# Kernel optimization log

Hardware: AMD Instinct MI355X
Metric: run time of the kernel (lower is better)

## Reference

```python
import jax, jax.numpy as jnp
import numpy as np

N_NODES = 50000
N_EDGES = 800000
IN_CH, OUT_CH, HEADS = 64, 32, 4
NEG_SLOPE = 0.2
BN_EPS = 1e-5


def setup_inputs() -> dict:
    key = jax.random.key(0)
    ks = jax.random.split(key, 9)
    x = jax.random.normal(ks[0], (N_NODES, IN_CH), dtype=jnp.float32)
    pos = jax.random.uniform(ks[1], (N_NODES, 3), dtype=jnp.float32)
    edge_index = jax.random.randint(ks[2], (2, N_EDGES), 0, N_NODES, dtype=jnp.int64)
    s = 1.0 / np.sqrt(IN_CH)
    W_l = jax.random.normal(ks[3], (IN_CH, HEADS * OUT_CH), dtype=jnp.float32) * s
    W_r = jax.random.normal(ks[4], (IN_CH, HEADS * OUT_CH), dtype=jnp.float32) * s
    W_edge = jax.random.normal(ks[5], (3, HEADS * OUT_CH), dtype=jnp.float32) * 0.5
    att = jax.random.normal(ks[6], (HEADS, OUT_CH), dtype=jnp.float32) * (1.0 / np.sqrt(OUT_CH))
    bn_gamma = jax.random.uniform(ks[7], (HEADS * OUT_CH,), dtype=jnp.float32, minval=0.5, maxval=1.5)
    bn_beta = jax.random.normal(ks[8], (HEADS * OUT_CH,), dtype=jnp.float32) * 0.1
    return {"x": x, "pos": pos, "edge_index": edge_index, "W_l": W_l, "W_r": W_r,
            "W_edge": W_edge, "att": att, "bn_gamma": bn_gamma, "bn_beta": bn_beta}


def reference(x, pos, edge_index, W_l, W_r, W_edge, att, bn_gamma, bn_beta):
    N = x.shape[0]
    H, C = att.shape
    # source->target projections (GATv2: lin_l for source/messages, lin_r for target)
    xl = (x @ W_l).reshape(N, H, C)
    xr = (x @ W_r).reshape(N, H, C)
    src, dst = edge_index[0], edge_index[1]
    edge_attr = pos[src] - pos[dst]  # [E,3] relative position as edge feature
    # add self-loops with fill_value='mean' (PyG default)
    loop = jnp.arange(N)
    src = jnp.concatenate([src, loop])
    dst = jnp.concatenate([dst, loop])
    mean_attr = edge_attr.mean(axis=0, keepdims=True)  # [1,3]
    edge_attr = jnp.concatenate([edge_attr, jnp.broadcast_to(mean_attr, (N, 3))], axis=0)
    # per-edge GATv2 score: att . LeakyReLU(x_l[j] + x_r[i] + W_e e_ij)
    e_feat = (edge_attr @ W_edge).reshape(-1, H, C)
    msg = xl[src]                              # [Et,H,C] (reused for aggregation)
    e = msg + xr[dst] + e_feat
    e = jax.nn.leaky_relu(e, NEG_SLOPE)
    score = jnp.einsum('ehc,hc->eh', e, att)   # [Et,H]
    # segment softmax over destination node
    m = jax.ops.segment_max(score, dst, num_segments=N)
    score = jnp.exp(score - m[dst])
    denom = jax.ops.segment_sum(score, dst, num_segments=N)
    alpha = score / (denom[dst] + 1e-16)       # [Et,H]
    out = jax.ops.segment_sum(alpha[:, :, None] * msg, dst, num_segments=N)
    out = out.reshape(N, H * C)
    # BatchNorm over node dimension (training-mode batch statistics, PyG BatchNorm)
    mu = out.mean(axis=0)
    var = out.var(axis=0)
    return (out - mu) / jnp.sqrt(var + BN_EPS) * bn_gamma + bn_beta
```

## Files before the change

kernel.cpp:

```cpp
#include <hip/hip_runtime.h>
#include <hip/hip_bf16.h>

#define N_NODES 50000
#define IN_CH 64
#define HC 128
#define CAP 64
#define NEG_SLOPE 0.2f
#define BN_EPS 1e-5f


__global__ __launch_bounds__(256) void k_gemm(const float* __restrict__ x,
                                              const float* __restrict__ Wl,
                                              const float* __restrict__ Wr,
                                              unsigned int* __restrict__ xl_bf,
                                              float* __restrict__ xr_out,
                                              int* __restrict__ deg,
                                              int* __restrict__ ocnt,
                                              float* __restrict__ mean_sums,
                                              float* __restrict__ bn_sums,
                                              int* __restrict__ flag,
                                              const int* __restrict__ eidx) {
  {
    int gtid = blockIdx.x * 256 + threadIdx.x;
    if (gtid < N_NODES) { deg[gtid] = 1; ocnt[gtid] = 0; }
    if (gtid < 256) bn_sums[gtid] = 0.f;
    if (gtid < 3) mean_sums[gtid] = 0.f;
    if (blockIdx.x == 0 && threadIdx.x < 64) {
      int w = eidx[2 * threadIdx.x + 1];
      unsigned long long nz = __ballot(w != 0);
      if (threadIdx.x == 0) flag[0] = (nz == 0ULL) ? 1 : 0;
    }
  }

  __shared__ float xs[16][IN_CH];
  __shared__ __hip_bfloat162 wsm[IN_CH][128];
  const int t = threadIdx.x;
  const int row0 = blockIdx.x * 16;

  for (int i = 0; i < 32; ++i) {
    int k = i * 2 + (t >> 7);
    int p = t & 127;
    int cc = p * 2;
    float2 wv;
    if (cc < 128) wv = *(const float2*)(Wl + k * 128 + cc);
    else          wv = *(const float2*)(Wr + k * 128 + (cc - 128));
    wsm[k][p] = __float22bfloat162_rn(wv);
  }
  {
    int r = t >> 4, c4 = (t & 15) * 4;
    *(float4*)&xs[r][c4] = *(const float4*)(x + (row0 + r) * IN_CH + c4);
  }
  __syncthreads();

  const int ct = t & 63;
  const int rt = t >> 6;
  const int c4 = ct * 4;
  const int r4 = rt * 4;

  float acc[4][4];
  #pragma unroll
  for (int a = 0; a < 4; ++a)
    #pragma unroll
    for (int b = 0; b < 4; ++b) acc[a][b] = 0.f;

  #pragma unroll 8
  for (int k = 0; k < IN_CH; ++k) {
    uint2 wraw = *(const uint2*)&wsm[k][ct * 2];
    float2 f01 = __bfloat1622float2(*(__hip_bfloat162*)&wraw.x);
    float2 f23 = __bfloat1622float2(*(__hip_bfloat162*)&wraw.y);
    float wv[4] = {f01.x, f01.y, f23.x, f23.y};
    float xv[4] = {xs[r4][k], xs[r4 + 1][k], xs[r4 + 2][k], xs[r4 + 3][k]};
    #pragma unroll
    for (int a = 0; a < 4; ++a)
      #pragma unroll
      for (int b = 0; b < 4; ++b) acc[a][b] = fmaf(xv[a], wv[b], acc[a][b]);
  }

  #pragma unroll
  for (int a = 0; a < 4; ++a) {
    int row = row0 + r4 + a;
    if (c4 < 128) {
      __hip_bfloat162 b01 = __float22bfloat162_rn(make_float2(acc[a][0], acc[a][1]));
      __hip_bfloat162 b23 = __float22bfloat162_rn(make_float2(acc[a][2], acc[a][3]));
      uint2 u;
      u.x = *(unsigned int*)&b01;
      u.y = *(unsigned int*)&b23;
      *(uint2*)(xl_bf + row * 64 + (c4 >> 1)) = u;
    } else {
      float4 v = make_float4(acc[a][0], acc[a][1], acc[a][2], acc[a][3]);
      *(float4*)(xr_out + row * HC + (c4 - 128)) = v;
    }
  }
}

__global__ __launch_bounds__(256) void k_edges(const int* __restrict__ eidx,
                                               int* __restrict__ deg,
                                               int* __restrict__ ocnt,
                                               int* __restrict__ srcs,
                                               const int* __restrict__ flag,
                                               int E) {
  const bool w64 = flag[0] != 0;
  const int stride = gridDim.x * blockDim.x;
  const int npair = (E + 1) >> 1;
  for (int e2 = blockIdx.x * blockDim.x + threadIdx.x; e2 < npair; e2 += stride) {
    int e0 = e2 * 2;
    bool has1 = (e0 + 1) < E;
    int s0, s1, d0, d1;
    if (w64) {
      int4 sv = *(const int4*)(eidx + 2 * e0);
      int4 dv = *(const int4*)(eidx + 2 * E + 2 * e0);
      s0 = sv.x; s1 = sv.z; d0 = dv.x; d1 = dv.z;
    } else {
      int2 sv = *(const int2*)(eidx + e0);
      int2 dv = *(const int2*)(eidx + E + e0);
      s0 = sv.x; s1 = sv.y; d0 = dv.x; d1 = dv.y;
    }
    int o0 = atomicAdd(&deg[d0], 1);
    if (o0 < CAP) srcs[d0 * CAP + o0] = s0;
    atomicAdd(&ocnt[s0], 1);
    if (has1) {
      int o1 = atomicAdd(&deg[d1], 1);
      if (o1 < CAP) srcs[d1 * CAP + o1] = s1;
      atomicAdd(&ocnt[s1], 1);
    }
  }
}

__global__ __launch_bounds__(256) void k_nodemean(const float* __restrict__ pos,
                                                  const int* __restrict__ deg,
                                                  const int* __restrict__ ocnt,
                                                  float* __restrict__ mean_sums) {
  float sx = 0.f, sy = 0.f, sz = 0.f;
  const int stride = gridDim.x * blockDim.x;
  for (int n = blockIdx.x * blockDim.x + threadIdx.x; n < N_NODES; n += stride) {
    float net = (float)(ocnt[n] - (deg[n] - 1));
    sx = fmaf(pos[3 * n],     net, sx);
    sy = fmaf(pos[3 * n + 1], net, sy);
    sz = fmaf(pos[3 * n + 2], net, sz);
  }
  #pragma unroll
  for (int m = 1; m < 64; m <<= 1) {
    sx += __shfl_xor(sx, m); sy += __shfl_xor(sy, m); sz += __shfl_xor(sz, m);
  }
  __shared__ float red[4][3];
  int wave = threadIdx.x >> 6, lane = threadIdx.x & 63;
  if (lane == 0) { red[wave][0] = sx; red[wave][1] = sy; red[wave][2] = sz; }
  __syncthreads();
  if (threadIdx.x == 0) {
    float a = 0.f, b = 0.f, c = 0.f;
    for (int w = 0; w < 4; ++w) { a += red[w][0]; b += red[w][1]; c += red[w][2]; }
    unsafeAtomicAdd(&mean_sums[0], a);
    unsafeAtomicAdd(&mean_sums[1], b);
    unsafeAtomicAdd(&mean_sums[2], c);
  }
}

__device__ __forceinline__ void edge4(int s, float dx, float dy, float dz, bool valid,
                                      const unsigned int* __restrict__ xl_bf, int l5,
                                      float4 xr4, float4 at4, float4 w0, float4 w1, float4 w2,
                                      float& a0, float& a1, float& a2, float& a3, float& den) {
  uint2 raw = *(const uint2*)(xl_bf + (s << 6) + (l5 << 1));
  float2 x01 = __bfloat1622float2(*(__hip_bfloat162*)&raw.x);
  float2 x23 = __bfloat1622float2(*(__hip_bfloat162*)&raw.y);
  float t0 = x01.x + xr4.x; t0 = fmaf(dx, w0.x, t0); t0 = fmaf(dy, w1.x, t0); t0 = fmaf(dz, w2.x, t0);
  float t1 = x01.y + xr4.y; t1 = fmaf(dx, w0.y, t1); t1 = fmaf(dy, w1.y, t1); t1 = fmaf(dz, w2.y, t1);
  float t2 = x23.x + xr4.z; t2 = fmaf(dx, w0.z, t2); t2 = fmaf(dy, w1.z, t2); t2 = fmaf(dz, w2.z, t2);
  float t3 = x23.y + xr4.w; t3 = fmaf(dx, w0.w, t3); t3 = fmaf(dy, w1.w, t3); t3 = fmaf(dz, w2.w, t3);
  float l0 = fmaf(NEG_SLOPE, fminf(t0, 0.f), fmaxf(t0, 0.f));
  float l1 = fmaf(NEG_SLOPE, fminf(t1, 0.f), fmaxf(t1, 0.f));
  float l2 = fmaf(NEG_SLOPE, fminf(t2, 0.f), fmaxf(t2, 0.f));
  float l3 = fmaf(NEG_SLOPE, fminf(t3, 0.f), fmaxf(t3, 0.f));
  float sc = l0 * at4.x;
  sc = fmaf(l1, at4.y, sc); sc = fmaf(l2, at4.z, sc); sc = fmaf(l3, at4.w, sc);
  sc += __shfl_xor(sc, 1); sc += __shfl_xor(sc, 2); sc += __shfl_xor(sc, 4);
  float e = __expf(sc);
  float p = valid ? e : 0.f;
  den += p;
  a0 = fmaf(p, x01.x, a0); a1 = fmaf(p, x01.y, a1);
  a2 = fmaf(p, x23.x, a2); a3 = fmaf(p, x23.y, a3);
}

__global__ __launch_bounds__(256) void k_agg(const unsigned int* __restrict__ xl_bf,
                                             float* __restrict__ xr_out,
                                             const float* __restrict__ pos,
                                             const float* __restrict__ att,
                                             const float* __restrict__ We,
                                             const float* __restrict__ mean_sums,
                                             const int* __restrict__ srcs,
                                             const int* __restrict__ deg,
                                             float invE) {
  const int lane = threadIdx.x & 63;
  const int half = lane >> 5;
  const int l5 = lane & 31;
  const int c = l5 << 2;

  const float4 at4 = *(const float4*)(att + c);
  const float4 w0 = *(const float4*)(We + c);
  const float4 w1 = *(const float4*)(We + 128 + c);
  const float4 w2 = *(const float4*)(We + 256 + c);
  const float m0 = mean_sums[0] * invE;
  const float m1 = mean_sums[1] * invE;
  const float m2 = mean_sums[2] * invE;

  const int gw = blockIdx.x * 4 + (threadIdx.x >> 6);
  const int W = gridDim.x * 4;

  for (int i = gw; i < N_NODES; i += W) {
    const float4 xr4 = *(const float4*)(xr_out + i * HC + c);
    const float px = pos[3 * i], py = pos[3 * i + 1], pz = pos[3 * i + 2];
    const int di = min(deg[i], CAP);
    const int sreg = srcs[i * CAP + lane];
    float a0 = 0.f, a1 = 0.f, a2 = 0.f, a3 = 0.f, den = 0.f;

    {
      int sA = __shfl(sreg, 1);
      if (half == 0) sA = i;
      bool vA = half < di;
      if (!vA) sA = i;
      int jB = 2 + half;
      int sB = __shfl(sreg, jB);
      bool vB = jB < di;
      if (!vB) sB = i;
      float pax = pos[3 * sA], pay = pos[3 * sA + 1], paz = pos[3 * sA + 2];
      float pbx = pos[3 * sB], pby = pos[3 * sB + 1], pbz = pos[3 * sB + 2];
      float dxA = (half == 0) ? m0 : pax - px;
      float dyA = (half == 0) ? m1 : pay - py;
      float dzA = (half == 0) ? m2 : paz - pz;
      edge4(sA, dxA, dyA, dzA, vA, xl_bf, l5, xr4, at4, w0, w1, w2, a0, a1, a2, a3, den);
      edge4(sB, pbx - px, pby - py, pbz - pz, vB, xl_bf, l5, xr4, at4, w0, w1, w2, a0, a1, a2, a3, den);
    }

    for (int j = 4; j < di; j += 4) {
      int jA = j + half;
      int jB = j + 2 + half;
      int sA = __shfl(sreg, jA);
      int sB = __shfl(sreg, jB);
      bool vA = jA < di;
      bool vB = jB < di;
      if (!vA) sA = i;
      if (!vB) sB = i;
      float pax = pos[3 * sA], pay = pos[3 * sA + 1], paz = pos[3 * sA + 2];
      float pbx = pos[3 * sB], pby = pos[3 * sB + 1], pbz = pos[3 * sB + 2];
      edge4(sA, pax - px, pay - py, paz - pz, vA, xl_bf, l5, xr4, at4, w0, w1, w2, a0, a1, a2, a3, den);
      edge4(sB, pbx - px, pby - py, pbz - pz, vB, xl_bf, l5, xr4, at4, w0, w1, w2, a0, a1, a2, a3, den);
    }

    den += __shfl_xor(den, 32);
    a0 += __shfl_xor(a0, 32);
    a1 += __shfl_xor(a1, 32);
    a2 += __shfl_xor(a2, 32);
    a3 += __shfl_xor(a3, 32);

    float inv = 1.f / (den + 1e-16f);
    if (half == 0) {
      float4 o = make_float4(a0 * inv, a1 * inv, a2 * inv, a3 * inv);
      *(float4*)(xr_out + i * HC + c) = o;
    }
  }
}

__global__ __launch_bounds__(128) void k_bnstats(const float* __restrict__ out,
                                                 float* __restrict__ bn_sums) {
  int c = threadIdx.x;
  float s = 0.f, ss = 0.f;
  int r = blockIdx.x;
  const int g = gridDim.x;
  for (; r + g < N_NODES; r += 2 * g) {
    float v0 = out[r * HC + c];
    float v1 = out[(r + g) * HC + c];
    s += v0; ss = fmaf(v0, v0, ss);
    s += v1; ss = fmaf(v1, v1, ss);
  }
  if (r < N_NODES) {
    float v = out[r * HC + c];
    s += v; ss = fmaf(v, v, ss);
  }
  unsafeAtomicAdd(&bn_sums[c], s);
  unsafeAtomicAdd(&bn_sums[128 + c], ss);
}

__global__ __launch_bounds__(256) void k_bnapply(float* __restrict__ out,
                                                 const float* __restrict__ bn_sums,
                                                 const float* __restrict__ gamma,
                                                 const float* __restrict__ beta,
                                                 int n4) {
  const int stride = gridDim.x * blockDim.x;
  const float invN = 1.f / (float)N_NODES;
  for (int i = blockIdx.x * blockDim.x + threadIdx.x; i < n4; i += stride) {
    int c = (i & 31) * 4;
    float4 v = ((float4*)out)[i];
    float4 s = *(const float4*)(bn_sums + c);
    float4 q = *(const float4*)(bn_sums + 128 + c);
    float4 g = *(const float4*)(gamma + c);
    float4 b = *(const float4*)(beta + c);
    float mu, var, rstd;
    mu = s.x * invN; var = q.x * invN - mu * mu; rstd = rsqrtf(var + BN_EPS);
    v.x = (v.x - mu) * rstd * g.x + b.x;
    mu = s.y * invN; var = q.y * invN - mu * mu; rstd = rsqrtf(var + BN_EPS);
    v.y = (v.y - mu) * rstd * g.y + b.y;
    mu = s.z * invN; var = q.z * invN - mu * mu; rstd = rsqrtf(var + BN_EPS);
    v.z = (v.z - mu) * rstd * g.z + b.z;
    mu = s.w * invN; var = q.w * invN - mu * mu; rstd = rsqrtf(var + BN_EPS);
    v.w = (v.w - mu) * rstd * g.w + b.w;
    ((float4*)out)[i] = v;
  }
}

extern "C" void kernel_launch(void* const* d_in, const int* in_sizes, int n_in,
                              void* d_out, int out_size, void* d_ws, size_t ws_size,
                              hipStream_t stream) {
  const float* x     = (const float*)d_in[0];
  const float* pos   = (const float*)d_in[1];
  const int*   eidx  = (const int*)d_in[2];
  const float* Wl    = (const float*)d_in[3];
  const float* Wr    = (const float*)d_in[4];
  const float* We    = (const float*)d_in[5];
  const float* att   = (const float*)d_in[6];
  const float* gamma = (const float*)d_in[7];
  const float* beta  = (const float*)d_in[8];
  float* out = (float*)d_out;
  const int E = in_sizes[2] / 2;

  char* ws = (char*)d_ws;
  int*   flag      = (int*)(ws + 0);
  float* mean_sums = (float*)(ws + 64);
  float* bn_sums   = (float*)(ws + 1024);
  int*   deg       = (int*)(ws + 4096);
  int*   ocnt      = (int*)(ws + (1 << 18));
  int*   srcs      = (int*)(ws + (1 << 19));
  unsigned int* xl_bf = (unsigned int*)(ws + (1 << 24));

  k_gemm<<<N_NODES / 16, 256, 0, stream>>>(x, Wl, Wr, xl_bf, out,
                                           deg, ocnt, mean_sums, bn_sums, flag, eidx);
  k_edges<<<1024, 256, 0, stream>>>(eidx, deg, ocnt, srcs, flag, E);
  k_nodemean<<<128, 256, 0, stream>>>(pos, deg, ocnt, mean_sums);
  k_agg<<<2048, 256, 0, stream>>>(xl_bf, out, pos, att, We, mean_sums, srcs, deg,
                                  1.f / (float)E);
  k_bnstats<<<512, 128, 0, stream>>>(out, bn_sums);
  k_bnapply<<<512, 256, 0, stream>>>(out, bn_sums, gamma, beta, out_size / 4);
}
```

Measured before the change: 288.9 us.

## Fuse edge-attr mean into edge scatter kernel, drop out-degree counting

The per-source out-count atomics and the separate node-mean kernel are removed. The edge kernel now accumulates pos[src]-pos[dst] directly and reduces it into mean_sums, with each thread handling 8 edges using vectorized index loads and batched atomics. This removes one atomic per edge and one kernel launch, at the cost of 6 random pos gathers per edge, and it changes the float summation order of the mean.

```diff
diff --git a/kernel.cpp b/kernel.cpp
--- a/kernel.cpp
+++ b/kernel.cpp
@@ -15,14 +15,13 @@
                                               unsigned int* __restrict__ xl_bf,
                                               float* __restrict__ xr_out,
                                               int* __restrict__ deg,
-                                              int* __restrict__ ocnt,
                                               float* __restrict__ mean_sums,
                                               float* __restrict__ bn_sums,
                                               int* __restrict__ flag,
                                               const int* __restrict__ eidx) {
   {
     int gtid = blockIdx.x * 256 + threadIdx.x;
-    if (gtid < N_NODES) { deg[gtid] = 1; ocnt[gtid] = 0; }
+    if (gtid < N_NODES) deg[gtid] = 1;
     if (gtid < 256) bn_sums[gtid] = 0.f;
     if (gtid < 3) mean_sums[gtid] = 0.f;
     if (blockIdx.x == 0 && threadIdx.x < 64) {
@@ -94,50 +93,62 @@
 }
 
 __global__ __launch_bounds__(256) void k_edges(const int* __restrict__ eidx,
+                                               const float* __restrict__ pos,
                                                int* __restrict__ deg,
-                                               int* __restrict__ ocnt,
                                                int* __restrict__ srcs,
+                                               float* __restrict__ mean_sums,
                                                const int* __restrict__ flag,
                                                int E) {
   const bool w64 = flag[0] != 0;
-  const int stride = gridDim.x * blockDim.x;
-  const int npair = (E + 1) >> 1;
-  for (int e2 = blockIdx.x * blockDim.x + threadIdx.x; e2 < npair; e2 += stride) {
-    int e0 = e2 * 2;
-    bool has1 = (e0 + 1) < E;
-    int s0, s1, d0, d1;
+  const int tid = blockIdx.x * 256 + threadIdx.x;
+  const int base = tid * 8;
+  float sx = 0.f, sy = 0.f, sz = 0.f;
+
+  const bool vec_ok = w64 ? ((E & 1) == 0) : ((E & 3) == 0);
+
+  if (base + 8 <= E && vec_ok) {
+    int s[8], d[8];
     if (w64) {
-      int4 sv = *(const int4*)(eidx + 2 * e0);
-      int4 dv = *(const int4*)(eidx + 2 * E + 2 * e0);
-      s0 = sv.x; s1 = sv.z; d0 = dv.x; d1 = dv.z;
+      const int4* ps = (const int4*)(eidx + 2 * base);
+      int4 A = ps[0], B = ps[1], C = ps[2], D = ps[3];
+      s[0]=A.x; s[1]=A.z; s[2]=B.x; s[3]=B.z; s[4]=C.x; s[5]=C.z; s[6]=D.x; s[7]=D.z;
+      const int4* pd = (const int4*)(eidx + 2 * E + 2 * base);
+      A = pd[0]; B = pd[1]; C = pd[2]; D = pd[3];
+      d[0]=A.x; d[1]=A.z; d[2]=B.x; d[3]=B.z; d[4]=C.x; d[5]=C.z; d[6]=D.x; d[7]=D.z;
     } else {
-      int2 sv = *(const int2*)(eidx + e0);
-      int2 dv = *(const int2*)(eidx + E + e0);
-      s0 = sv.x; s1 = sv.y; d0 = dv.x; d1 = dv.y;
-    }
-    int o0 = atomicAdd(&deg[d0], 1);
-    if (o0 < CAP) srcs[d0 * CAP + o0] = s0;
-    atomicAdd(&ocnt[s0], 1);
-    if (has1) {
-      int o1 = atomicAdd(&deg[d1], 1);
-      if (o1 < CAP) srcs[d1 * CAP + o1] = s1;
-      atomicAdd(&ocnt[s1], 1);
-    }
-  }
-}
-
-__global__ __launch_bounds__(256) void k_nodemean(const float* __restrict__ pos,
-                                                  const int* __restrict__ deg,
-                                                  const int* __restrict__ ocnt,
-                                                  float* __restrict__ mean_sums) {
-  float sx = 0.f, sy = 0.f, sz = 0.f;
-  const int stride = gridDim.x * blockDim.x;
-  for (int n = blockIdx.x * blockDim.x + threadIdx.x; n < N_NODES; n += stride) {
-    float net = (float)(ocnt[n] - (deg[n] - 1));
-    sx = fmaf(pos[3 * n],     net, sx);
-    sy = fmaf(pos[3 * n + 1], net, sy);
-    sz = fmaf(pos[3 * n + 2], net, sz);
-  }
+      int4 A = *(const int4*)(eidx + base);
+      int4 B = *(const int4*)(eidx + base + 4);
+      s[0]=A.x; s[1]=A.y; s[2]=A.z; s[3]=A.w; s[4]=B.x; s[5]=B.y; s[6]=B.z; s[7]=B.w;
+      A = *(const int4*)(eidx + E + base);
+      B = *(const int4*)(eidx + E + base + 4);
+      d[0]=A.x; d[1]=A.y; d[2]=A.z; d[3]=A.w; d[4]=B.x; d[5]=B.y; d[6]=B.z; d[7]=B.w;
+    }
+    int slot[8];
+    #pragma unroll
+    for (int k = 0; k < 8; ++k) slot[k] = atomicAdd(&deg[d[k]], 1);
+    #pragma unroll
+    for (int k = 0; k < 8; ++k)
+      if (slot[k] < CAP) srcs[d[k] * CAP + slot[k]] = s[k];
+    #pragma unroll
+    for (int k = 0; k < 8; ++k) {
+      sx += pos[3 * s[k]]     - pos[3 * d[k]];
+      sy += pos[3 * s[k] + 1] - pos[3 * d[k] + 1];
+      sz += pos[3 * s[k] + 2] - pos[3 * d[k] + 2];
+    }
+  } else if (base < E) {
+    int hi = min(base + 8, E);
+    for (int e = base; e < hi; ++e) {
+      int s, d;
+      if (w64) { s = eidx[2 * e]; d = eidx[2 * (E + e)]; }
+      else     { s = eidx[e];     d = eidx[E + e]; }
+      int o = atomicAdd(&deg[d], 1);
+      if (o < CAP) srcs[d * CAP + o] = s;
+      sx += pos[3 * s]     - pos[3 * d];
+      sy += pos[3 * s + 1] - pos[3 * d + 1];
+      sz += pos[3 * s + 2] - pos[3 * d + 2];
+    }
+  }
+
   #pragma unroll
   for (int m = 1; m < 64; m <<= 1) {
     sx += __shfl_xor(sx, m); sy += __shfl_xor(sy, m); sz += __shfl_xor(sz, m);
@@ -326,14 +337,13 @@
   float* mean_sums = (float*)(ws + 64);
   float* bn_sums   = (float*)(ws + 1024);
   int*   deg       = (int*)(ws + 4096);
-  int*   ocnt      = (int*)(ws + (1 << 18));
   int*   srcs      = (int*)(ws + (1 << 19));
   unsigned int* xl_bf = (unsigned int*)(ws + (1 << 24));
 
   k_gemm<<<N_NODES / 16, 256, 0, stream>>>(x, Wl, Wr, xl_bf, out,
-                                           deg, ocnt, mean_sums, bn_sums, flag, eidx);
-  k_edges<<<1024, 256, 0, stream>>>(eidx, deg, ocnt, srcs, flag, E);
-  k_nodemean<<<128, 256, 0, stream>>>(pos, deg, ocnt, mean_sums);
+                                           deg, mean_sums, bn_sums, flag, eidx);
+  int eblocks = (E + 2047) / 2048;
+  k_edges<<<eblocks, 256, 0, stream>>>(eidx, pos, deg, srcs, mean_sums, flag, E);
   k_agg<<<2048, 256, 0, stream>>>(xl_bf, out, pos, att, We, mean_sums, srcs, deg,
                                   1.f / (float)E);
   k_bnstats<<<512, 128, 0, stream>>>(out, bn_sums);
```

Result: faster. 256.6 us (-11.2%).
